# Kernel optimization log

Hardware: AMD Instinct MI355X
Metric: run time of the kernel (lower is better)

The kernel has to match this reference:

```python
import jax, jax.numpy as jnp
import numpy as np

N_NODES = 16000
N_EDGES = 256000
F = 128        # invariant edge feature dim
MUL = 64       # multiplicity of env/V irreps (mul_gcd)
HID = 128      # mlp_n_hidden
SQRT3 = float(np.sqrt(3.0))

# e3nn-style activation normalization constant for silu:
# c = sqrt(E_{z~N(0,1)}[silu(z)^2]), so silu(z)/c has unit second moment.
_z = np.linspace(-12.0, 12.0, 100001)
_pdf = np.exp(-0.5 * _z ** 2) / np.sqrt(2.0 * np.pi)
_silu = _z / (1.0 + np.exp(-_z))
SILU_C = float(np.sqrt(np.trapz(_silu ** 2 * _pdf, _z)))


def _nsilu(x):
    return jax.nn.silu(x) / SILU_C


def _lin(x, W):
    # e3nn 'path' gradient normalization: W ~ N(0,1), forward scaled by 1/sqrt(fan_in)
    return (x @ W) / jnp.sqrt(jnp.asarray(W.shape[0], x.dtype))


def setup_inputs() -> dict:
    key = jax.random.key(0)
    ks = jax.random.split(key, 11)
    inp = {
        'vectors': jax.random.normal(ks[0], (N_EDGES, 3), jnp.float32),
        'x': jax.random.normal(ks[1], (N_EDGES, F), jnp.float32),
        'V': jax.random.normal(ks[2], (N_EDGES, 4 * MUL), jnp.float32),  # 64x0e + 64x1o
        'u': jax.random.uniform(ks[3], (N_EDGES,), jnp.float32),
        'm': jnp.ones((N_EDGES,), jnp.float32),
        'W_env': jax.random.normal(ks[4], (F, 2 * MUL), jnp.float32),
        'W1': jax.random.normal(ks[5], (F + 2 * MUL, HID), jnp.float32),
        'W2': jax.random.normal(ks[6], (HID, HID), jnp.float32),
        'W3': jax.random.normal(ks[7], (HID, HID), jnp.float32),
        'W_out': jax.random.normal(ks[8], (2 * MUL, MUL), jnp.float32),
        'senders': jax.random.randint(ks[9], (N_EDGES,), 0, N_NODES, jnp.int32),
    }
    return inp


def reference(vectors, x, V, u, m, W_env, W1, W2, W3, W_out, senders):
    E = vectors.shape[0]
    x = x * m[:, None]

    # n_neighbors = scatter_sum(m, dst=senders, map_back=True)
    n_neighbors = jax.ops.segment_sum(m, senders, num_segments=N_NODES)[senders]  # (E,)

    # w = Linear(num_irreps=2*MUL)(x)
    w = _lin(x, W_env)                  # (E, 128)
    w0, w1 = w[:, :MUL], w[:, MUL:]     # scalar / vector channel weights

    # spherical harmonics (component normalization): Y0 = 1, Y1 = sqrt(3)*rhat
    rhat = vectors / jnp.linalg.norm(vectors, axis=-1, keepdims=True)
    Y1 = SQRT3 * rhat                   # (E, 3)

    # w * Y * m, scatter_sum over senders, map back, normalize by n_neighbors
    denom = n_neighbors + 1e-5
    ws = w0 * m[:, None]                                   # (E, MUL)   w * Y0
    wv = (w1[:, :, None] * Y1[:, None, :]) * m[:, None, None]  # (E, MUL, 3)
    wY_s = jax.ops.segment_sum(ws, senders, num_segments=N_NODES)[senders] / denom[:, None]
    wY_v = jax.ops.segment_sum(wv, senders, num_segments=N_NODES)[senders] / denom[:, None, None]

    # V.mul_to_axis(): (E, MUL, 0e+1o)
    Vs = V[:, :MUL]                      # (E, MUL)
    Vv = V[:, MUL:].reshape(E, MUL, 3)   # (E, MUL, 3)

    # tensor product, filter_ir_out = {0e, 1o} (CG, component normalization)
    s_a = wY_s * Vs                                  # 0e x 0e -> 0e
    s_b = jnp.sum(wY_v * Vv, axis=-1) / SQRT3        # 1o x 1o -> 0e
    v_a = wY_s[:, :, None] * Vv                      # 0e x 1o -> 1o
    v_b = wY_v * Vs[:, :, None]                      # 1o x 0e -> 1o

    # scalars -> concatenated into x; vectors stay equivariant
    x = jnp.concatenate([x, s_a, s_b], axis=1)       # (E, F + 2*MUL)

    # invariant MLP (silu, no output activation)
    h = _nsilu(_lin(x, W1))
    h = _nsilu(_lin(h, W2))
    h = _lin(h, W3)                                  # (E, HID)
    x_out = u[:, None] * h

    # Linear(irreps_out=64x1o) on 128x1o
    V_in = jnp.concatenate([v_a, v_b], axis=1)       # (E, 2*MUL, 3)
    V_out = jnp.einsum('euk,uo->eok', V_in, W_out) / jnp.sqrt(jnp.asarray(2 * MUL, V.dtype))
    V_out = V_out.reshape(E, MUL * 3)                # (E, 192)

    return x_out, V_out
```

## Files before the change

### kernel.cpp

```cpp
#include <hip/hip_runtime.h>
#include <math.h>

typedef short bf16x8 __attribute__((ext_vector_type(8)));
typedef float f32x4 __attribute__((ext_vector_type(4)));

#define S128 0.08838834764831845f
#define S256I 0.0625f
#define NN_NODES 16000

#define WS_COUNTS   16448000
#define WS_OFFSETS  (WS_COUNTS + 64000)
#define WS_CURSOR   (WS_OFFSETS + 64000)
#define WS_ORDER    (WS_CURSOR + 64000)
#define WS_W1 (WS_ORDER + 1024000)
#define WS_W2 (WS_W1 + 65536)
#define WS_W3 (WS_W2 + 32768)
#define WS_WO (WS_W3 + 32768)
#define WS_WE (WS_WO + 16384)

static float compute_inv_silu_c() {
    double sum = 0.0, prev = 0.0;
    const double dz = 24.0 / 100000.0;
    for (int i = 0; i <= 100000; ++i) {
        double z = -12.0 + dz * (double)i;
        double pdf = exp(-0.5 * z * z) * 0.3989422804014327;
        double s = z / (1.0 + exp(-z));
        double f = s * s * pdf;
        if (i) sum += 0.5 * (prev + f) * dz;
        prev = f;
    }
    return (float)(1.0 / sqrt(sum));
}
static const float INV_SILU_C = compute_inv_silu_c();

__device__ __forceinline__ unsigned int packbf(float a, float b) {
    union { float f; unsigned int u; } ca, cb;
    ca.f = a; cb.f = b;
    unsigned int ua = ca.u + (0x7fffu + ((ca.u >> 16) & 1u));
    unsigned int ub = cb.u + (0x7fffu + ((cb.u >> 16) & 1u));
    return (ua >> 16) | (ub & 0xffff0000u);
}
__device__ __forceinline__ unsigned short bf16r(float v) {
    union { float f; unsigned int u; } c; c.f = v;
    return (unsigned short)((c.u + (0x7fffu + ((c.u >> 16) & 1u))) >> 16);
}
__device__ __forceinline__ float bflo(unsigned int u) { return __uint_as_float(u << 16); }
__device__ __forceinline__ float bfhi(unsigned int u) { return __uint_as_float(u & 0xffff0000u); }
__device__ __forceinline__ int swz(int row, int b) { return b ^ ((row & 7) << 4); }
__device__ __forceinline__ float nsilu(float v, float ic) {
    return v / (1.0f + __expf(-v)) * ic;
}

__global__ __launch_bounds__(256) void k_wprep(
    const float* __restrict__ W1, const float* __restrict__ W2,
    const float* __restrict__ W3, const float* __restrict__ Wout,
    const float* __restrict__ Wenv, char* __restrict__ wsb)
{
    const int t = blockIdx.x * 256 + threadIdx.x;
    if (t < 32768) {
        int n = t & 127, k = t >> 7;
        *(unsigned short*)(wsb + WS_W1 + n * 512 + ((k * 2) ^ ((n & 7) << 4))) =
            bf16r(W1[k * 128 + n] * S256I);
    }
    if (t < 16384) {
        int n = t & 127, k = t >> 7;
        *(unsigned short*)(wsb + WS_W2 + n * 256 + ((k * 2) ^ ((n & 7) << 4))) =
            bf16r(W2[k * 128 + n] * S128);
        *(unsigned short*)(wsb + WS_W3 + n * 256 + ((k * 2) ^ ((n & 7) << 4))) =
            bf16r(W3[k * 128 + n] * S128);
    }
    if (t < 16384) {
        int j = t & 127, k = t >> 7;
        int c = (j & 1) ? 64 + (j >> 1) : (j >> 1);
        *(unsigned short*)(wsb + WS_WE + j * 256 + ((k * 2) ^ ((j & 7) << 4))) =
            bf16r(Wenv[k * 128 + c] * S128);
    }
    if (t < 8192) {
        int o = t & 63, uu = t >> 6;
        *(unsigned short*)(wsb + WS_WO + o * 256 + ((uu * 2) ^ ((o & 7) << 4))) =
            bf16r(Wout[uu * 64 + o] * S128);
    }
}

__global__ __launch_bounds__(1024) void k_hist(
    const int* __restrict__ senders, int* __restrict__ counts, int E)
{
    const int e = blockIdx.x * 1024 + threadIdx.x;
    if (e < E) atomicAdd(&counts[senders[e]], 1);
}

__global__ __launch_bounds__(1024) void k_scan(
    const int* __restrict__ counts, int* __restrict__ offsets,
    int* __restrict__ cursor)
{
    __shared__ int part[1024];
    const int t = threadIdx.x;
    const int s0 = t * 16;
    const int s1 = (s0 + 16 < NN_NODES) ? s0 + 16 : NN_NODES;
    int s = 0;
    for (int i = s0; i < s1; ++i) s += counts[i];
    part[t] = s;
    __syncthreads();
    for (int off = 1; off < 1024; off <<= 1) {
        int v = part[t];
        if (t >= off) v += part[t - off];
        __syncthreads();
        part[t] = v;
        __syncthreads();
    }
    int run = t ? part[t - 1] : 0;
    for (int i = s0; i < s1; ++i) {
        offsets[i] = run; cursor[i] = run; run += counts[i];
    }
}

__global__ __launch_bounds__(1024) void k_binfill(
    const int* __restrict__ senders, int* __restrict__ cursor,
    int* __restrict__ order, int E)
{
    const int e = blockIdx.x * 1024 + threadIdx.x;
    if (e < E) {
        const int p = atomicAdd(&cursor[senders[e]], 1);
        order[p] = e;
    }
}

__global__ __launch_bounds__(512) void k_env(
    const float* __restrict__ x, const float* __restrict__ m,
    const char* __restrict__ wsb, char* __restrict__ wout, int E)
{
    __shared__ char lds[65536];
    const int tid = threadIdx.x;

    {
        const int4* src = (const int4*)(wsb + WS_WE);
        int4* dst = (int4*)(lds + 32768);
        #pragma unroll
        for (int j = 0; j < 4; ++j) dst[tid * 4 + j] = src[tid * 4 + j];
    }

    const int eb = blockIdx.x * 128;
    {
        const int el = tid >> 2, q = tid & 3;
        const int e = eb + el;
        if (e < E) {
            const float mv = m[e];
            const float4* xp = (const float4*)&x[(size_t)e * 128 + q * 32];
            #pragma unroll
            for (int j = 0; j < 4; ++j) {
                float4 A = xp[2 * j], B = xp[2 * j + 1];
                int4 w;
                w.x = packbf(A.x * mv, A.y * mv); w.y = packbf(A.z * mv, A.w * mv);
                w.z = packbf(B.x * mv, B.y * mv); w.w = packbf(B.z * mv, B.w * mv);
                *(int4*)(lds + el * 256 + swz(el, q * 64 + j * 16)) = w;
            }
        } else {
            const int4 z = {0, 0, 0, 0};
            #pragma unroll
            for (int j = 0; j < 4; ++j)
                *(int4*)(lds + el * 256 + swz(el, q * 64 + j * 16)) = z;
        }
    }
    __syncthreads();

    const int l = tid & 63, wid = tid >> 6;
    const int wm = wid & 3, wn = wid >> 2;
    const int m0 = wm * 32, n0 = wn * 64;
    const int lr = l & 15, lg = l >> 4;

    f32x4 acc[2][4];
    #pragma unroll
    for (int a = 0; a < 2; ++a)
        #pragma unroll
        for (int b = 0; b < 4; ++b) acc[a][b] = (f32x4){0.f, 0.f, 0.f, 0.f};

    #pragma unroll
    for (int kk = 0; kk < 4; ++kk) {
        const int kb = kk * 64 + lg * 16;
        bf16x8 a0 = *(const bf16x8*)(lds + (m0 + lr) * 256      + swz(m0 + lr, kb));
        bf16x8 a1 = *(const bf16x8*)(lds + (m0 + 16 + lr) * 256 + swz(m0 + 16 + lr, kb));
        #pragma unroll
        for (int nt = 0; nt < 4; ++nt) {
            const int row = n0 + nt * 16 + lr;
            bf16x8 bb = *(const bf16x8*)(lds + 32768 + row * 256 + swz(row, kb));
            acc[0][nt] = __builtin_amdgcn_mfma_f32_16x16x32_bf16(a0, bb, acc[0][nt], 0, 0, 0);
            acc[1][nt] = __builtin_amdgcn_mfma_f32_16x16x32_bf16(a1, bb, acc[1][nt], 0, 0, 0);
        }
    }
    __syncthreads();

    #pragma unroll
    for (int mt = 0; mt < 2; ++mt)
        #pragma unroll
        for (int nt = 0; nt < 4; ++nt)
            #pragma unroll
            for (int r = 0; r < 4; ++r) {
                const int row = m0 + mt * 16 + lg * 4 + r;
                const int col = n0 + nt * 16 + lr;
                *(unsigned short*)(lds + row * 256 + col * 2) = bf16r(acc[mt][nt][r]);
            }
    __syncthreads();
    {
        const int4* s = (const int4*)lds;
        int4* d = (int4*)(wout + (size_t)eb * 256);
        #pragma unroll
        for (int j = 0; j < 4; ++j) d[tid * 4 + j] = s[tid * 4 + j];
    }
}

__global__ __launch_bounds__(256) void k_gather(
    const char* __restrict__ wvb, const float* __restrict__ vectors,
    const float* __restrict__ m, const int* __restrict__ counts,
    const int* __restrict__ offsets, const int* __restrict__ order,
    float* __restrict__ node_cnt, float* __restrict__ node_s,
    float* __restrict__ node_v)
{
    const int l = threadIdx.x & 63, wid = threadIdx.x >> 6;
    const int n = blockIdx.x * 4 + wid;
    if (n >= NN_NODES) return;
    const int cnt = counts[n], base = offsets[n];

    float as = 0.f, a0 = 0.f, a1 = 0.f, a2 = 0.f, am = 0.f;
    for (int i = 0; i < cnt; ++i) {
        const int e = order[base + i];
        const unsigned int wv = *(const unsigned int*)(wvb + (size_t)e * 256 + l * 4);
        const float mm = m[e];
        const float vx = vectors[(size_t)e * 3 + 0];
        const float vy = vectors[(size_t)e * 3 + 1];
        const float vz = vectors[(size_t)e * 3 + 2];
        const float rn = 1.7320508075688772f / sqrtf(vx * vx + vy * vy + vz * vz);
        const float w0 = bflo(wv) * mm;
        const float c1 = bfhi(wv) * mm * rn;
        as += w0; am += mm;
        a0 += c1 * vx; a1 += c1 * vy; a2 += c1 * vz;
    }
    if (l == 0) node_cnt[n] = am;
    node_s[(size_t)n * 64 + l] = as;
    float* nv = &node_v[((size_t)n * 64 + l) * 3];
    nv[0] = a0; nv[1] = a1; nv[2] = a2;
}

__global__ __launch_bounds__(512) void k_prep_vout(
    const float* __restrict__ V, const int* __restrict__ senders,
    const float* __restrict__ node_cnt, const float* __restrict__ node_s,
    const float* __restrict__ node_v, const char* __restrict__ wsb,
    float* __restrict__ out_x, float* __restrict__ out_v, int E)
{
    __shared__ char lds[49152 + 16384];
    const int tid = threadIdx.x, l = tid & 63, wid = tid >> 6;

    {
        const int4* src = (const int4*)(wsb + WS_WO);
        int4 a = src[tid * 2], b = src[tid * 2 + 1];
        ((int4*)(lds + 49152))[tid * 2]     = a;
        ((int4*)(lds + 49152))[tid * 2 + 1] = b;
    }

    const int eb = blockIdx.x * 64;
    #pragma unroll 2
    for (int i = 0; i < 8; ++i) {
        const int el = wid * 8 + i;
        const int e  = eb + el;
        float Vs = 0.f, Vv0 = 0.f, Vv1 = 0.f, Vv2 = 0.f;
        float wYs = 0.f, wv0 = 0.f, wv1 = 0.f, wv2 = 0.f;
        if (e < E) {
            Vs = V[(size_t)e * 256 + l];
            const float* vp = &V[(size_t)e * 256 + 64 + l * 3];
            Vv0 = vp[0]; Vv1 = vp[1]; Vv2 = vp[2];
            const int sn = senders[e];
            const float rden = 1.0f / (node_cnt[sn] + 1e-5f);
            wYs = node_s[(size_t)sn * 64 + l] * rden;
            const float* nvp = &node_v[((size_t)sn * 64 + l) * 3];
            wv0 = nvp[0] * rden; wv1 = nvp[1] * rden; wv2 = nvp[2] * rden;
            unsigned short* sab = (unsigned short*)((char*)out_x + (size_t)e * 512);
            sab[l]      = bf16r(wYs * Vs);
            sab[64 + l] = bf16r((wv0 * Vv0 + wv1 * Vv1 + wv2 * Vv2) * 0.57735026918962576f);
        }
        const float vvk[3] = {Vv0, Vv1, Vv2};
        const float wvk[3] = {wv0, wv1, wv2};
        #pragma unroll
        for (int k = 0; k < 3; ++k) {
            const int row = el * 3 + k;
            *(unsigned short*)(lds + row * 256 + swz(row, l * 2))       = bf16r(wYs * vvk[k]);
            *(unsigned short*)(lds + row * 256 + swz(row, 128 + l * 2)) = bf16r(wvk[k] * Vs);
        }
    }
    __syncthreads();

    const int wm = wid & 3, wn = wid >> 2;
    const int m0 = wm * 48, n0 = wn * 32;
    const int lr = l & 15, lg = l >> 4;
    f32x4 acc[3][2];
    #pragma unroll
    for (int a = 0; a < 3; ++a)
        #pragma unroll
        for (int b = 0; b < 2; ++b) acc[a][b] = (f32x4){0.f, 0.f, 0.f, 0.f};

    #pragma unroll
    for (int kk = 0; kk < 4; ++kk) {
        const int kb = kk * 64 + lg * 16;
        bf16x8 a0 = *(const bf16x8*)(lds + (m0 + lr) * 256      + swz(m0 + lr, kb));
        bf16x8 a1 = *(const bf16x8*)(lds + (m0 + 16 + lr) * 256 + swz(m0 + 16 + lr, kb));
        bf16x8 a2 = *(const bf16x8*)(lds + (m0 + 32 + lr) * 256 + swz(m0 + 32 + lr, kb));
        bf16x8 b0 = *(const bf16x8*)(lds + 49152 + (n0 + lr) * 256      + swz(n0 + lr, kb));
        bf16x8 b1 = *(const bf16x8*)(lds + 49152 + (n0 + 16 + lr) * 256 + swz(n0 + 16 + lr, kb));
        acc[0][0] = __builtin_amdgcn_mfma_f32_16x16x32_bf16(a0, b0, acc[0][0], 0, 0, 0);
        acc[0][1] = __builtin_amdgcn_mfma_f32_16x16x32_bf16(a0, b1, acc[0][1], 0, 0, 0);
        acc[1][0] = __builtin_amdgcn_mfma_f32_16x16x32_bf16(a1, b0, acc[1][0], 0, 0, 0);
        acc[1][1] = __builtin_amdgcn_mfma_f32_16x16x32_bf16(a1, b1, acc[1][1], 0, 0, 0);
        acc[2][0] = __builtin_amdgcn_mfma_f32_16x16x32_bf16(a2, b0, acc[2][0], 0, 0, 0);
        acc[2][1] = __builtin_amdgcn_mfma_f32_16x16x32_bf16(a2, b1, acc[2][1], 0, 0, 0);
    }

    #pragma unroll
    for (int mt = 0; mt < 3; ++mt)
        #pragma unroll
        for (int nt = 0; nt < 2; ++nt)
            #pragma unroll
            for (int r = 0; r < 4; ++r) {
                const int mm = m0 + mt * 16 + lg * 4 + r;
                const int el2 = mm / 3, kd = mm - el2 * 3;
                const int e = eb + el2;
                const int o = n0 + nt * 16 + lr;
                if (e < E) out_v[(size_t)e * 192 + o * 3 + kd] = acc[mt][nt][r];
            }
}

__global__ __launch_bounds__(512) void k_mlp(
    const float* __restrict__ x, const float* __restrict__ m,
    const float* __restrict__ ug, const char* __restrict__ wsb,
    float* __restrict__ out_x, float inv_c, int E)
{
    __shared__ char lds0[65536];
    __shared__ char lds1[65536];
    const int tid = threadIdx.x;

    {
        const int4* src = (const int4*)(wsb + WS_W1);
        int4* dst = (int4*)lds1;
        #pragma unroll
        for (int j = 0; j < 8; ++j) dst[tid * 8 + j] = src[tid * 8 + j];
    }

    const int eb = blockIdx.x * 128;
    {
        const int el = tid >> 2, q = tid & 3;
        const int e  = eb + el;
        if (e < E) {
            const float mv = m[e];
            const float4* xp = (const float4*)&x[(size_t)e * 128 + q * 32];
            #pragma unroll
            for (int j = 0; j < 4; ++j) {
                float4 A = xp[2 * j], B = xp[2 * j + 1];
                int4 w;
                w.x = packbf(A.x * mv, A.y * mv); w.y = packbf(A.z * mv, A.w * mv);
                w.z = packbf(B.x * mv, B.y * mv); w.w = packbf(B.z * mv, B.w * mv);
                *(int4*)(lds0 + el * 512 + swz(el, q * 64 + j * 16)) = w;
            }
            const int4* sp = (const int4*)((const char*)out_x + (size_t)e * 512 + q * 64);
            #pragma unroll
            for (int j = 0; j < 4; ++j) {
                int4 v = sp[j];
                *(int4*)(lds0 + el * 512 + swz(el, 256 + q * 64 + j * 16)) = v;
            }
        } else {
            const int4 z = {0, 0, 0, 0};
            #pragma unroll
            for (int j = 0; j < 4; ++j) {
                *(int4*)(lds0 + el * 512 + swz(el, q * 64 + j * 16)) = z;
                *(int4*)(lds0 + el * 512 + swz(el, 256 + q * 64 + j * 16)) = z;
            }
        }
    }
    __syncthreads();

    const int l = tid & 63, wid = tid >> 6;
    const int wm = wid >> 1, wn = wid & 1;
    const int m0 = wm * 32, n0 = wn * 64;
    const int lr = l & 15, lg = l >> 4;

    f32x4 acc[2][4];
    #pragma unroll
    for (int a = 0; a < 2; ++a)
        #pragma unroll
        for (int b = 0; b < 4; ++b) acc[a][b] = (f32x4){0.f, 0.f, 0.f, 0.f};
    #pragma unroll 2
    for (int kk = 0; kk < 8; ++kk) {
        const int kb = kk * 64 + lg * 16;
        bf16x8 a0 = *(const bf16x8*)(lds0 + (m0 + lr) * 512      + swz(m0 + lr, kb));
        bf16x8 a1 = *(const bf16x8*)(lds0 + (m0 + 16 + lr) * 512 + swz(m0 + 16 + lr, kb));
        #pragma unroll
        for (int nt = 0; nt < 4; ++nt) {
            const int row = n0 + nt * 16 + lr;
            bf16x8 bb = *(const bf16x8*)(lds1 + row * 512 + swz(row, kb));
            acc[0][nt] = __builtin_amdgcn_mfma_f32_16x16x32_bf16(a0, bb, acc[0][nt], 0, 0, 0);
            acc[1][nt] = __builtin_amdgcn_mfma_f32_16x16x32_bf16(a1, bb, acc[1][nt], 0, 0, 0);
        }
    }

    int4 r2[4], r3[4];
    {
        const int4* s2 = (const int4*)(wsb + WS_W2);
        const int4* s3 = (const int4*)(wsb + WS_W3);
        #pragma unroll
        for (int j = 0; j < 4; ++j) { r2[j] = s2[tid * 4 + j]; r3[j] = s3[tid * 4 + j]; }
    }
    __syncthreads();

    #pragma unroll
    for (int mt = 0; mt < 2; ++mt)
        #pragma unroll
        for (int nt = 0; nt < 4; ++nt)
            #pragma unroll
            for (int r = 0; r < 4; ++r) {
                const int row = m0 + mt * 16 + lg * 4 + r;
                const int col = n0 + nt * 16 + lr;
                *(unsigned short*)(lds0 + row * 256 + swz(row, col * 2)) =
                    bf16r(nsilu(acc[mt][nt][r], inv_c));
            }
    {
        int4* d2 = (int4*)(lds0 + 32768);
        int4* d3 = (int4*)lds1;
        #pragma unroll
        for (int j = 0; j < 4; ++j) { d2[tid * 4 + j] = r2[j]; d3[tid * 4 + j] = r3[j]; }
    }
    __syncthreads();

    f32x4 acc2[2][4];
    #pragma unroll
    for (int a = 0; a < 2; ++a)
        #pragma unroll
        for (int b = 0; b < 4; ++b) acc2[a][b] = (f32x4){0.f, 0.f, 0.f, 0.f};
    #pragma unroll
    for (int kk = 0; kk < 4; ++kk) {
        const int kb = kk * 64 + lg * 16;
        bf16x8 a0 = *(const bf16x8*)(lds0 + (m0 + lr) * 256      + swz(m0 + lr, kb));
        bf16x8 a1 = *(const bf16x8*)(lds0 + (m0 + 16 + lr) * 256 + swz(m0 + 16 + lr, kb));
        #pragma unroll
        for (int nt = 0; nt < 4; ++nt) {
            const int row = n0 + nt * 16 + lr;
            bf16x8 bb = *(const bf16x8*)(lds0 + 32768 + row * 256 + swz(row, kb));
            acc2[0][nt] = __builtin_amdgcn_mfma_f32_16x16x32_bf16(a0, bb, acc2[0][nt], 0, 0, 0);
            acc2[1][nt] = __builtin_amdgcn_mfma_f32_16x16x32_bf16(a1, bb, acc2[1][nt], 0, 0, 0);
        }
    }
    #pragma unroll
    for (int mt = 0; mt < 2; ++mt)
        #pragma unroll
        for (int nt = 0; nt < 4; ++nt)
            #pragma unroll
            for (int r = 0; r < 4; ++r) {
                const int row = m0 + mt * 16 + lg * 4 + r;
                const int col = n0 + nt * 16 + lr;
                *(unsigned short*)(lds1 + 32768 + row * 256 + swz(row, col * 2)) =
                    bf16r(nsilu(acc2[mt][nt][r], inv_c));
            }
    __syncthreads();

    f32x4 acc3[2][4];
    #pragma unroll
    for (int a = 0; a < 2; ++a)
        #pragma unroll
        for (int b = 0; b < 4; ++b) acc3[a][b] = (f32x4){0.f, 0.f, 0.f, 0.f};
    #pragma unroll
    for (int kk = 0; kk < 4; ++kk) {
        const int kb = kk * 64 + lg * 16;
        bf16x8 a0 = *(const bf16x8*)(lds1 + 32768 + (m0 + lr) * 256      + swz(m0 + lr, kb));
        bf16x8 a1 = *(const bf16x8*)(lds1 + 32768 + (m0 + 16 + lr) * 256 + swz(m0 + 16 + lr, kb));
        #pragma unroll
        for (int nt = 0; nt < 4; ++nt) {
            const int row = n0 + nt * 16 + lr;
            bf16x8 bb = *(const bf16x8*)(lds1 + row * 256 + swz(row, kb));
            acc3[0][nt] = __builtin_amdgcn_mfma_f32_16x16x32_bf16(a0, bb, acc3[0][nt], 0, 0, 0);
            acc3[1][nt] = __builtin_amdgcn_mfma_f32_16x16x32_bf16(a1, bb, acc3[1][nt], 0, 0, 0);
        }
    }
    #pragma unroll
    for (int mt = 0; mt < 2; ++mt)
        #pragma unroll
        for (int r = 0; r < 4; ++r) {
            const int e = eb + m0 + mt * 16 + lg * 4 + r;
            if (e < E) {
                const float uu = ug[e];
                #pragma unroll
                for (int nt = 0; nt < 4; ++nt)
                    out_x[(size_t)e * 128 + n0 + nt * 16 + lr] = uu * acc3[mt][nt][r];
            }
        }
}

extern "C" void kernel_launch(void* const* d_in, const int* in_sizes, int n_in,
                              void* d_out, int out_size, void* d_ws, size_t ws_size,
                              hipStream_t stream) {
    const float* vectors = (const float*)d_in[0];
    const float* x       = (const float*)d_in[1];
    const float* V       = (const float*)d_in[2];
    const float* u       = (const float*)d_in[3];
    const float* m       = (const float*)d_in[4];
    const float* W_env   = (const float*)d_in[5];
    const float* W1      = (const float*)d_in[6];
    const float* W2      = (const float*)d_in[7];
    const float* W3      = (const float*)d_in[8];
    const float* W_out   = (const float*)d_in[9];
    const int*   senders = (const int*)d_in[10];

    const int E = in_sizes[4];

    char*  wsb      = (char*)d_ws;
    float* node_cnt = (float*)d_ws;
    float* node_s   = node_cnt + NN_NODES;
    float* node_v   = node_s + (size_t)NN_NODES * 64;
    int* counts  = (int*)(wsb + WS_COUNTS);
    int* offsets = (int*)(wsb + WS_OFFSETS);
    int* cursor  = (int*)(wsb + WS_CURSOR);
    int* order   = (int*)(wsb + WS_ORDER);

    float* out_x = (float*)d_out;
    float* out_v = out_x + (size_t)E * 128;
    char*  wvb   = (char*)out_v;

    hipMemsetAsync(counts, 0, 64000, stream);

    k_wprep<<<128, 256, 0, stream>>>(W1, W2, W3, W_out, W_env, wsb);
    k_hist<<<(E + 1023) / 1024, 1024, 0, stream>>>(senders, counts, E);
    k_scan<<<1, 1024, 0, stream>>>(counts, offsets, cursor);
    k_binfill<<<(E + 1023) / 1024, 1024, 0, stream>>>(senders, cursor, order, E);
    k_env<<<(E + 127) / 128, 512, 0, stream>>>(x, m, wsb, wvb, E);
    k_gather<<<(NN_NODES + 3) / 4, 256, 0, stream>>>(wvb, vectors, m, counts,
                                                     offsets, order,
                                                     node_cnt, node_s, node_v);
    k_prep_vout<<<(E + 63) / 64, 512, 0, stream>>>(V, senders, node_cnt, node_s,
                                                   node_v, wsb, out_x, out_v, E);
    k_mlp<<<(E + 127) / 128, 512, 0, stream>>>(x, m, u, wsb, out_x, INV_SILU_C, E);
}
```

Measured before the change: 496.6 us.

## Read MLP weights from global/L2, halve k_mlp LDS, stage V_out stores, fold memset

k_mlp now reads the W1/W2/W3 B-operands straight from global memory, stored unswizzled, instead of copying them into LDS. This halves the shared memory per block to 64 KB, and launch bounds ask for more resident blocks to raise occupancy. The V_out kernel now stages its output tile in LDS and writes it back with coalesced int4 stores instead of scattered 4-byte stores. The counts memset is folded into k_wprep, removing a separate API call. The trade-off is that the weight reads now depend on L1/L2 hit rates and global memory latency, where before they came from LDS.

```diff
diff --git a/kernel.cpp b/kernel.cpp
--- a/kernel.cpp
+++ b/kernel.cpp
@@ -57,16 +57,17 @@
     const float* __restrict__ Wenv, char* __restrict__ wsb)
 {
     const int t = blockIdx.x * 256 + threadIdx.x;
+    if (t < NN_NODES) ((int*)(wsb + WS_COUNTS))[t] = 0;
     if (t < 32768) {
         int n = t & 127, k = t >> 7;
-        *(unsigned short*)(wsb + WS_W1 + n * 512 + ((k * 2) ^ ((n & 7) << 4))) =
+        *(unsigned short*)(wsb + WS_W1 + n * 512 + k * 2) =
             bf16r(W1[k * 128 + n] * S256I);
     }
     if (t < 16384) {
         int n = t & 127, k = t >> 7;
-        *(unsigned short*)(wsb + WS_W2 + n * 256 + ((k * 2) ^ ((n & 7) << 4))) =
+        *(unsigned short*)(wsb + WS_W2 + n * 256 + k * 2) =
             bf16r(W2[k * 128 + n] * S128);
-        *(unsigned short*)(wsb + WS_W3 + n * 256 + ((k * 2) ^ ((n & 7) << 4))) =
+        *(unsigned short*)(wsb + WS_W3 + n * 256 + k * 2) =
             bf16r(W3[k * 128 + n] * S128);
     }
     if (t < 16384) {
@@ -311,6 +312,7 @@
         acc[2][0] = __builtin_amdgcn_mfma_f32_16x16x32_bf16(a2, b0, acc[2][0], 0, 0, 0);
         acc[2][1] = __builtin_amdgcn_mfma_f32_16x16x32_bf16(a2, b1, acc[2][1], 0, 0, 0);
     }
+    __syncthreads();
 
     #pragma unroll
     for (int mt = 0; mt < 3; ++mt)
@@ -320,27 +322,31 @@
             for (int r = 0; r < 4; ++r) {
                 const int mm = m0 + mt * 16 + lg * 4 + r;
                 const int el2 = mm / 3, kd = mm - el2 * 3;
-                const int e = eb + el2;
                 const int o = n0 + nt * 16 + lr;
-                if (e < E) out_v[(size_t)e * 192 + o * 3 + kd] = acc[mt][nt][r];
-            }
-}
-
-__global__ __launch_bounds__(512) void k_mlp(
+                *(float*)(lds + el2 * 768 + (o * 3 + kd) * 4) = acc[mt][nt][r];
+            }
+    __syncthreads();
+    if (eb + 64 <= E) {
+        const int4* s = (const int4*)lds;
+        int4* d = (int4*)(out_v + (size_t)eb * 192);
+        #pragma unroll
+        for (int j = 0; j < 6; ++j) d[tid * 6 + j] = s[tid * 6 + j];
+    } else {
+        for (int idx = tid; idx < 64 * 192; idx += 512) {
+            const int el2 = idx / 192;
+            if (eb + el2 < E)
+                out_v[(size_t)(eb + el2) * 192 + (idx % 192)] = *(float*)(lds + idx * 4);
+        }
+    }
+}
+
+__global__ __launch_bounds__(512, 4) void k_mlp(
     const float* __restrict__ x, const float* __restrict__ m,
     const float* __restrict__ ug, const char* __restrict__ wsb,
     float* __restrict__ out_x, float inv_c, int E)
 {
-    __shared__ char lds0[65536];
-    __shared__ char lds1[65536];
+    __shared__ char lds[65536];
     const int tid = threadIdx.x;
-
-    {
-        const int4* src = (const int4*)(wsb + WS_W1);
-        int4* dst = (int4*)lds1;
-        #pragma unroll
-        for (int j = 0; j < 8; ++j) dst[tid * 8 + j] = src[tid * 8 + j];
-    }
 
     const int eb = blockIdx.x * 128;
     {
@@ -355,20 +361,20 @@
                 int4 w;
                 w.x = packbf(A.x * mv, A.y * mv); w.y = packbf(A.z * mv, A.w * mv);
                 w.z = packbf(B.x * mv, B.y * mv); w.w = packbf(B.z * mv, B.w * mv);
-                *(int4*)(lds0 + el * 512 + swz(el, q * 64 + j * 16)) = w;
+                *(int4*)(lds + el * 512 + swz(el, q * 64 + j * 16)) = w;
             }
             const int4* sp = (const int4*)((const char*)out_x + (size_t)e * 512 + q * 64);
             #pragma unroll
             for (int j = 0; j < 4; ++j) {
                 int4 v = sp[j];
-                *(int4*)(lds0 + el * 512 + swz(el, 256 + q * 64 + j * 16)) = v;
+                *(int4*)(lds + el * 512 + swz(el, 256 + q * 64 + j * 16)) = v;
             }
         } else {
             const int4 z = {0, 0, 0, 0};
             #pragma unroll
             for (int j = 0; j < 4; ++j) {
-                *(int4*)(lds0 + el * 512 + swz(el, q * 64 + j * 16)) = z;
-                *(int4*)(lds0 + el * 512 + swz(el, 256 + q * 64 + j * 16)) = z;
+                *(int4*)(lds + el * 512 + swz(el, q * 64 + j * 16)) = z;
+                *(int4*)(lds + el * 512 + swz(el, 256 + q * 64 + j * 16)) = z;
             }
         }
     }
@@ -379,6 +385,10 @@
     const int m0 = wm * 32, n0 = wn * 64;
     const int lr = l & 15, lg = l >> 4;
 
+    const char* w1g = wsb + WS_W1;
+    const char* w2g = wsb + WS_W2;
+    const char* w3g = wsb + WS_W3;
+
     f32x4 acc[2][4];
     #pragma unroll
     for (int a = 0; a < 2; ++a)
@@ -387,23 +397,15 @@
     #pragma unroll 2
     for (int kk = 0; kk < 8; ++kk) {
         const int kb = kk * 64 + lg * 16;
-        bf16x8 a0 = *(const bf16x8*)(lds0 + (m0 + lr) * 512      + swz(m0 + lr, kb));
-        bf16x8 a1 = *(const bf16x8*)(lds0 + (m0 + 16 + lr) * 512 + swz(m0 + 16 + lr, kb));
+        bf16x8 a0 = *(const bf16x8*)(lds + (m0 + lr) * 512      + swz(m0 + lr, kb));
+        bf16x8 a1 = *(const bf16x8*)(lds + (m0 + 16 + lr) * 512 + swz(m0 + 16 + lr, kb));
         #pragma unroll
         for (int nt = 0; nt < 4; ++nt) {
             const int row = n0 + nt * 16 + lr;
-            bf16x8 bb = *(const bf16x8*)(lds1 + row * 512 + swz(row, kb));
+            bf16x8 bb = *(const bf16x8*)(w1g + row * 512 + kb);
             acc[0][nt] = __builtin_amdgcn_mfma_f32_16x16x32_bf16(a0, bb, acc[0][nt], 0, 0, 0);
             acc[1][nt] = __builtin_amdgcn_mfma_f32_16x16x32_bf16(a1, bb, acc[1][nt], 0, 0, 0);
         }
-    }
-
-    int4 r2[4], r3[4];
-    {
-        const int4* s2 = (const int4*)(wsb + WS_W2);
-        const int4* s3 = (const int4*)(wsb + WS_W3);
-        #pragma unroll
-        for (int j = 0; j < 4; ++j) { r2[j] = s2[tid * 4 + j]; r3[j] = s3[tid * 4 + j]; }
     }
     __syncthreads();
 
@@ -415,15 +417,9 @@
             for (int r = 0; r < 4; ++r) {
                 const int row = m0 + mt * 16 + lg * 4 + r;
                 const int col = n0 + nt * 16 + lr;
-                *(unsigned short*)(lds0 + row * 256 + swz(row, col * 2)) =
+                *(unsigned short*)(lds + row * 256 + swz(row, col * 2)) =
                     bf16r(nsilu(acc[mt][nt][r], inv_c));
             }
-    {
-        int4* d2 = (int4*)(lds0 + 32768);
-        int4* d3 = (int4*)lds1;
-        #pragma unroll
-        for (int j = 0; j < 4; ++j) { d2[tid * 4 + j] = r2[j]; d3[tid * 4 + j] = r3[j]; }
-    }
     __syncthreads();
 
     f32x4 acc2[2][4];
@@ -434,12 +430,12 @@
     #pragma unroll
     for (int kk = 0; kk < 4; ++kk) {
         const int kb = kk * 64 + lg * 16;
-        bf16x8 a0 = *(const bf16x8*)(lds0 + (m0 + lr) * 256      + swz(m0 + lr, kb));
-        bf16x8 a1 = *(const bf16x8*)(lds0 + (m0 + 16 + lr) * 256 + swz(m0 + 16 + lr, kb));
+        bf16x8 a0 = *(const bf16x8*)(lds + (m0 + lr) * 256      + swz(m0 + lr, kb));
+        bf16x8 a1 = *(const bf16x8*)(lds + (m0 + 16 + lr) * 256 + swz(m0 + 16 + lr, kb));
         #pragma unroll
         for (int nt = 0; nt < 4; ++nt) {
             const int row = n0 + nt * 16 + lr;
-            bf16x8 bb = *(const bf16x8*)(lds0 + 32768 + row * 256 + swz(row, kb));
+            bf16x8 bb = *(const bf16x8*)(w2g + row * 256 + kb);
             acc2[0][nt] = __builtin_amdgcn_mfma_f32_16x16x32_bf16(a0, bb, acc2[0][nt], 0, 0, 0);
             acc2[1][nt] = __builtin_amdgcn_mfma_f32_16x16x32_bf16(a1, bb, acc2[1][nt], 0, 0, 0);
         }
@@ -452,7 +448,7 @@
             for (int r = 0; r < 4; ++r) {
                 const int row = m0 + mt * 16 + lg * 4 + r;
                 const int col = n0 + nt * 16 + lr;
-                *(unsigned short*)(lds1 + 32768 + row * 256 + swz(row, col * 2)) =
+                *(unsigned short*)(lds + 32768 + row * 256 + swz(row, col * 2)) =
                     bf16r(nsilu(acc2[mt][nt][r], inv_c));
             }
     __syncthreads();
@@ -465,12 +461,12 @@
     #pragma unroll
     for (int kk = 0; kk < 4; ++kk) {
         const int kb = kk * 64 + lg * 16;
-        bf16x8 a0 = *(const bf16x8*)(lds1 + 32768 + (m0 + lr) * 256      + swz(m0 + lr, kb));
-        bf16x8 a1 = *(const bf16x8*)(lds1 + 32768 + (m0 + 16 + lr) * 256 + swz(m0 + 16 + lr, kb));
+        bf16x8 a0 = *(const bf16x8*)(lds + 32768 + (m0 + lr) * 256      + swz(m0 + lr, kb));
+        bf16x8 a1 = *(const bf16x8*)(lds + 32768 + (m0 + 16 + lr) * 256 + swz(m0 + 16 + lr, kb));
         #pragma unroll
         for (int nt = 0; nt < 4; ++nt) {
             const int row = n0 + nt * 16 + lr;
-            bf16x8 bb = *(const bf16x8*)(lds1 + row * 256 + swz(row, kb));
+            bf16x8 bb = *(const bf16x8*)(w3g + row * 256 + kb);
             acc3[0][nt] = __builtin_amdgcn_mfma_f32_16x16x32_bf16(a0, bb, acc3[0][nt], 0, 0, 0);
             acc3[1][nt] = __builtin_amdgcn_mfma_f32_16x16x32_bf16(a1, bb, acc3[1][nt], 0, 0, 0);
         }
@@ -519,8 +515,6 @@
     float* out_v = out_x + (size_t)E * 128;
     char*  wvb   = (char*)out_v;
 
-    hipMemsetAsync(counts, 0, 64000, stream);
-
     k_wprep<<<128, 256, 0, stream>>>(W1, W2, W3, W_out, W_env, wsb);
     k_hist<<<(E + 1023) / 1024, 1024, 0, stream>>>(senders, counts, E);
     k_scan<<<1, 1024, 0, stream>>>(counts, offsets, cursor);
```

Result: slower. 507.4 us (+2.2%).
